# Performance work log

Hardware: AMD Instinct MI355X
Metric: run time of the kernel (lower is better)

## Reference

```python
import jax, jax.numpy as jnp
import numpy as np

CHUNK = 64  # rows of `a` processed per step to bound the [chunk, N, d] abs-diff intermediate
TAIL_K = 4          # selection_tail_size
FAR_K = 64          # far_sample_count
PUSH_K = 4          # pushing_sample_size
HUBER_DELTA = 1.0   # torch.nn.HuberLoss default


def cdist_l1(a, b):
    # a: [M, d], b: [N, d] -> [M, N] Manhattan distances, computed in row chunks
    M, d = a.shape
    def f(a_chunk):  # [CHUNK, d] -> [CHUNK, N]
        return jnp.abs(a_chunk[:, None, :] - b[None, :, :]).sum(-1)
    return jax.lax.map(f, a.reshape(-1, CHUNK, d)).reshape(M, b.shape[0])


def smallest_k_mean(dists, k):
    # mean of the k smallest entries along last dim
    neg_vals, _ = jax.lax.top_k(-dists, k)
    return (-neg_vals).mean(-1)


def huber(x):
    # HuberLoss(pred=x, target=0), delta=1
    ax = jnp.abs(x)
    return jnp.where(ax < HUBER_DELTA, 0.5 * x * x, HUBER_DELTA * (ax - 0.5 * HUBER_DELTA))


def setup_inputs() -> dict:
    key = jax.random.key(0)
    k1, k2 = jax.random.split(key)
    space_samples = jax.random.normal(k1, (2048, 256), dtype=jnp.float32)
    latents = jax.random.normal(k2, (8192, 256), dtype=jnp.float32)
    return {"space_samples": space_samples, "latents": latents}


def reference(space_samples, latents):
    # space_samples: [M, d] drawn from latent_sampler; latents: [N, d]
    space_dists = cdist_l1(space_samples, latents)            # [M, N]
    tail_dists = smallest_k_mean(space_dists, TAIL_K)          # [M]
    far_inds = jax.lax.top_k(tail_dists, FAR_K)[1]             # [FAR_K]
    far_samples = space_samples[far_inds]                      # [FAR_K, d]
    empty_dists = cdist_l1(far_samples, latents)               # [FAR_K, N]
    close_dists = smallest_k_mean(empty_dists, PUSH_K)         # [FAR_K]
    return huber(close_dists).mean()
```

## Files before the change

kernel.cpp:

```cpp
#include <hip/hip_runtime.h>
#include <hip/hip_bf16.h>


static constexpr int M = 2048;
static constexpr int N = 8192;
static constexpr int KQ = 64;
static constexpr int BKQ = 16;
static constexpr int ROWS_PER_BLK = 128;
static constexpr int COLS_PER_BLK = 128;
static constexpr int NCHUNK = N / COLS_PER_BLK;

static constexpr float QS  = 21.0f;
static constexpr float QB  = 126.0f;
static constexpr float INV_QS = 1.0f / 21.0f;

__device__ __forceinline__ float med3f(float a, float b, float c) {
    return __builtin_amdgcn_fmed3f(a, b, c);
}

__device__ __forceinline__ void ins4(float d, float& s0, float& s1, float& s2, float& s3) {
    float n0 = fminf(s0, d);
    float n1 = med3f(s0, s1, d);
    float n2 = med3f(s1, s2, d);
    float n3 = med3f(s2, s3, d);
    s0 = n0; s1 = n1; s2 = n2; s3 = n3;
}

__device__ __forceinline__ unsigned int sad8(unsigned int a, unsigned int b, unsigned int c) {
#if __has_builtin(__builtin_amdgcn_sad_u8)
    return __builtin_amdgcn_sad_u8(a, b, c);
#else
    unsigned int d;
    asm("v_sad_u8 %0, %1, %2, %3" : "=v"(d) : "v"(a), "v"(b), "v"(c));
    return d;
#endif
}

__device__ __forceinline__ unsigned int quant4(const float4 v) {
    const float y0 = fminf(fmaxf(fmaf(v.x, QS, QB), 0.0f), 255.0f);
    const float y1 = fminf(fmaxf(fmaf(v.y, QS, QB), 0.0f), 255.0f);
    const float y2 = fminf(fmaxf(fmaf(v.z, QS, QB), 0.0f), 255.0f);
    const float y3 = fminf(fmaxf(fmaf(v.w, QS, QB), 0.0f), 255.0f);
    const unsigned int b0 = (unsigned int)(int)rintf(y0);
    const unsigned int b1 = (unsigned int)(int)rintf(y1);
    const unsigned int b2 = (unsigned int)(int)rintf(y2);
    const unsigned int b3 = (unsigned int)(int)rintf(y3);
    return b0 | (b1 << 8) | (b2 << 16) | (b3 << 24);
}

__device__ __forceinline__ float huber_pos(float x) {
    const float ax = __builtin_fabsf(x);
    return (ax < 1.0f) ? (0.5f * x * x) : (ax - 0.5f);
}

__global__ __launch_bounds__(256)
void convert_kernel(const float* __restrict__ A, const float* __restrict__ B,
                    unsigned int* __restrict__ At, unsigned int* __restrict__ Bt) {
    __shared__ unsigned int lt[KQ * 65];
    const int tid = threadIdx.x;
    const bool isB = (blockIdx.x < N / 64);
    const float* src = isB ? B : A;
    unsigned int* dst = isB ? Bt : At;
    const int rows = isB ? N : M;
    const int r0 = (isB ? blockIdx.x : (blockIdx.x - N / 64)) * 64;

#pragma unroll
    for (int it = 0; it < 16; ++it) {
        const int qi = it * 256 + tid;
        const int row = qi >> 6;
        const int kq = qi & 63;
        const float4 v = *(const float4*)&src[(r0 + row) * 256 + 4 * kq];
        lt[kq * 65 + row] = quant4(v);
    }
    __syncthreads();
#pragma unroll
    for (int it = 0; it < 16; ++it) {
        const int wi = it * 256 + tid;
        const int row = wi & 63;
        const int kq = wi >> 6;
        dst[(size_t)kq * rows + r0 + row] = lt[kq * 65 + row];
    }
}

__global__ __launch_bounds__(256, 4)
void dist4_kernel(const unsigned int* __restrict__ At, const unsigned int* __restrict__ Bt,
                  float4* __restrict__ ws_dist) {
    __shared__ __align__(16) unsigned int tiles[8192];
    const int tid = threadIdx.x;
    const int tx = tid & 15;
    const int ty = tid >> 4;
    const int bx = blockIdx.x;
    const int by = blockIdx.y;
    const int rowBase = by * ROWS_PER_BLK;
    const int colBase = bx * COLS_PER_BLK;

    const int sKq = tid >> 5;
    const int sC  = (tid & 31) * 4;

    unsigned int acc[8][8];
#pragma unroll
    for (int i = 0; i < 8; ++i)
#pragma unroll
        for (int j = 0; j < 8; ++j) acc[i][j] = 0u;

    uint4 pa0, pa1, pb0, pb1;
    pa0 = *(const uint4*)&At[(sKq) * M + rowBase + sC];
    pa1 = *(const uint4*)&At[(sKq + 8) * M + rowBase + sC];
    pb0 = *(const uint4*)&Bt[(sKq) * N + colBase + sC];
    pb1 = *(const uint4*)&Bt[(sKq + 8) * N + colBase + sC];
    {
        unsigned int* As = tiles;
        unsigned int* Bs = tiles + 2048;
        *(uint4*)&As[sKq * 128 + sC] = pa0;
        *(uint4*)&As[(sKq + 8) * 128 + sC] = pa1;
        *(uint4*)&Bs[sKq * 128 + sC] = pb0;
        *(uint4*)&Bs[(sKq + 8) * 128 + sC] = pb1;
    }

    for (int t0 = 0; t0 < KQ / BKQ; ++t0) {
        __syncthreads();
        if (t0 + 1 < KQ / BKQ) {
            const int kb = (t0 + 1) * BKQ;
            pa0 = *(const uint4*)&At[(kb + sKq) * M + rowBase + sC];
            pa1 = *(const uint4*)&At[(kb + sKq + 8) * M + rowBase + sC];
            pb0 = *(const uint4*)&Bt[(kb + sKq) * N + colBase + sC];
            pb1 = *(const uint4*)&Bt[(kb + sKq + 8) * N + colBase + sC];
        }

        const unsigned int* As = tiles + (t0 & 1) * 4096;
        const unsigned int* Bs = As + 2048;
#pragma unroll 4
        for (int kq = 0; kq < BKQ; ++kq) {
            const uint4 aw0 = *(const uint4*)&As[kq * 128 + 8 * ty];
            const uint4 aw1 = *(const uint4*)&As[kq * 128 + 8 * ty + 4];
            const uint4 bw0 = *(const uint4*)&Bs[kq * 128 + 4 * tx];
            const uint4 bw1 = *(const uint4*)&Bs[kq * 128 + 64 + 4 * tx];
            const unsigned int a[8] = {aw0.x, aw0.y, aw0.z, aw0.w, aw1.x, aw1.y, aw1.z, aw1.w};
            const unsigned int b[8] = {bw0.x, bw0.y, bw0.z, bw0.w, bw1.x, bw1.y, bw1.z, bw1.w};
#pragma unroll
            for (int i = 0; i < 8; ++i) {
#pragma unroll
                for (int j = 0; j < 8; ++j) {
                    acc[i][j] = sad8(a[i], b[j], acc[i][j]);
                }
            }
        }

        if (t0 + 1 < KQ / BKQ) {
            __syncthreads();
            unsigned int* Asw = tiles + ((t0 + 1) & 1) * 4096;
            unsigned int* Bsw = Asw + 2048;
            *(uint4*)&Asw[sKq * 128 + sC] = pa0;
            *(uint4*)&Asw[(sKq + 8) * 128 + sC] = pa1;
            *(uint4*)&Bsw[sKq * 128 + sC] = pb0;
            *(uint4*)&Bsw[(sKq + 8) * 128 + sC] = pb1;
        }
    }

    float s[8][4];
#pragma unroll
    for (int i = 0; i < 8; ++i) {
        float s0 = 1e30f, s1 = 1e30f, s2 = 1e30f, s3 = 1e30f;
#pragma unroll
        for (int j = 0; j < 8; ++j) {
            const float d = (float)acc[i][j] * INV_QS;
            ins4(d, s0, s1, s2, s3);
        }
        s[i][0] = s0; s[i][1] = s1; s[i][2] = s2; s[i][3] = s3;
    }

#pragma unroll
    for (int lvl = 1; lvl <= 8; lvl <<= 1) {
#pragma unroll
        for (int i = 0; i < 8; ++i) {
            const float o0 = __shfl_xor(s[i][0], lvl, 64);
            const float o1 = __shfl_xor(s[i][1], lvl, 64);
            const float o2 = __shfl_xor(s[i][2], lvl, 64);
            const float o3 = __shfl_xor(s[i][3], lvl, 64);
            ins4(o0, s[i][0], s[i][1], s[i][2], s[i][3]);
            ins4(o1, s[i][0], s[i][1], s[i][2], s[i][3]);
            ins4(o2, s[i][0], s[i][1], s[i][2], s[i][3]);
            ins4(o3, s[i][0], s[i][1], s[i][2], s[i][3]);
        }
    }

    if (tx == 0) {
#pragma unroll
        for (int i = 0; i < 8; ++i) {
            ws_dist[bx * M + rowBase + 8 * ty + i] =
                make_float4(s[i][0], s[i][1], s[i][2], s[i][3]);
        }
    }
}

__global__ __launch_bounds__(256)
void tail_kernel(const float4* __restrict__ ws_dist, float* __restrict__ tail) {
    const int gtid = blockIdx.x * 256 + threadIdx.x;
    const int row = gtid >> 3;
    const int q = gtid & 7;
    float s0 = 1e30f, s1 = 1e30f, s2 = 1e30f, s3 = 1e30f;
#pragma unroll
    for (int c = 0; c < 8; ++c) {
        const float4 v = ws_dist[(q * 8 + c) * M + row];
        ins4(v.x, s0, s1, s2, s3);
        ins4(v.y, s0, s1, s2, s3);
        ins4(v.z, s0, s1, s2, s3);
        ins4(v.w, s0, s1, s2, s3);
    }
#pragma unroll
    for (int lvl = 1; lvl <= 4; lvl <<= 1) {
        const float o0 = __shfl_xor(s0, lvl, 64);
        const float o1 = __shfl_xor(s1, lvl, 64);
        const float o2 = __shfl_xor(s2, lvl, 64);
        const float o3 = __shfl_xor(s3, lvl, 64);
        ins4(o0, s0, s1, s2, s3);
        ins4(o1, s0, s1, s2, s3);
        ins4(o2, s0, s1, s2, s3);
        ins4(o3, s0, s1, s2, s3);
    }
    if (q == 0) tail[row] = (s0 + s1 + s2 + s3) * 0.25f;
}

__global__ __launch_bounds__(1024)
void top64_kernel(const float* __restrict__ tail, float* __restrict__ out) {
    __shared__ unsigned int hist[8][256];
    __shared__ unsigned int ctrl[2];
    __shared__ float wsum[16];
    __shared__ unsigned int wcnt[16];
    const int tid = threadIdx.x;
    const int wid = tid >> 6;
    const int lane = tid & 63;

    const unsigned int k0 = __float_as_uint(tail[tid]);
    const unsigned int k1 = __float_as_uint(tail[tid + 1024]);

    if (tid == 0) { ctrl[0] = 0u; ctrl[1] = 64u; }

    for (int p = 0; p < 4; ++p) {
        const int shift = 24 - 8 * p;
        ((unsigned int*)hist)[tid] = 0u;
        ((unsigned int*)hist)[tid + 1024] = 0u;
        __syncthreads();
        const unsigned int prefix = ctrl[0];
        const unsigned int t = ctrl[1];
        bool c0 = true, c1 = true;
        if (p > 0) {
            const int sh8 = shift + 8;
            c0 = ((k0 >> sh8) == (prefix >> sh8));
            c1 = ((k1 >> sh8) == (prefix >> sh8));
        }
        if (c0) atomicAdd(&hist[wid & 7][(k0 >> shift) & 255], 1u);
        if (c1) atomicAdd(&hist[wid & 7][(k1 >> shift) & 255], 1u);
        __syncthreads();
        if (tid < 256) {
            unsigned int h = 0;
#pragma unroll
            for (int r = 0; r < 8; ++r) h += hist[r][tid];
            hist[0][tid] = h;
        }
        __syncthreads();
        if (wid == 0) {
            const unsigned int s4 = hist[0][4 * lane] + hist[0][4 * lane + 1] +
                                    hist[0][4 * lane + 2] + hist[0][4 * lane + 3];
            unsigned int suf = s4;
#pragma unroll
            for (int off = 1; off < 64; off <<= 1) {
                const unsigned int v = __shfl_down(suf, off, 64);
                if (lane + off < 64) suf += v;
            }
            const unsigned long long mask = __ballot(suf >= t);
            const int lstar = 63 - __clzll(mask);
            if (lane == lstar) {
                unsigned int c = suf - s4;
                for (int d = 4 * lstar + 3; d >= 4 * lstar; --d) {
                    const unsigned int cd = hist[0][d];
                    c += cd;
                    if (c >= t) {
                        ctrl[0] = prefix | ((unsigned int)d << shift);
                        ctrl[1] = t - (c - cd);
                        break;
                    }
                }
            }
        }
        __syncthreads();
    }

    const unsigned int T = ctrl[0];
    float sum = 0.0f;
    unsigned int cnt = 0;
    if (k0 > T) { ++cnt; sum += huber_pos(__uint_as_float(k0)); }
    if (k1 > T) { ++cnt; sum += huber_pos(__uint_as_float(k1)); }
#pragma unroll
    for (int off = 32; off > 0; off >>= 1) {
        sum += __shfl_down(sum, off, 64);
        cnt += __shfl_down(cnt, off, 64);
    }
    if (lane == 0) { wsum[wid] = sum; wcnt[wid] = cnt; }
    __syncthreads();
    if (tid == 0) {
        float S = 0.0f;
        unsigned int C = 0;
#pragma unroll
        for (int w = 0; w < 16; ++w) { S += wsum[w]; C += wcnt[w]; }
        const float hT = huber_pos(__uint_as_float(T));
        out[0] = (S + (float)(64u - C) * hT) * (1.0f / 64.0f);
    }
}

extern "C" void kernel_launch(void* const* d_in, const int* in_sizes, int n_in,
                              void* d_out, int out_size, void* d_ws, size_t ws_size,
                              hipStream_t stream) {
    const float* A = (const float*)d_in[0];
    const float* B = (const float*)d_in[1];
    float* out = (float*)d_out;

    unsigned int* Bt = (unsigned int*)d_ws;
    unsigned int* At = (unsigned int*)((char*)d_ws + (size_t)KQ * N * 4);
    float4* ws_dist = (float4*)((char*)d_ws + (size_t)KQ * N * 4 + (size_t)KQ * M * 4);
    float* tail = (float*)((char*)ws_dist + (size_t)NCHUNK * M * sizeof(float4));

    convert_kernel<<<dim3(N / 64 + M / 64), 256, 0, stream>>>(A, B, At, Bt);
    dist4_kernel<<<dim3(NCHUNK, M / ROWS_PER_BLK), 256, 0, stream>>>(At, Bt, ws_dist);
    tail_kernel<<<dim3(M * 8 / 256), 256, 0, stream>>>(ws_dist, tail);
    top64_kernel<<<1, 1024, 0, stream>>>(tail, out);
}
```

Before: 122.4 us.

## Fuse four kernels into one persistent kernel with global atomic barriers

Merges the convert, distance, tail and top-64 kernels into a single launch over 1024 blocks, separated by software grid barriers built on agent-scope atomics, plus a memset to reset the barrier counters. The aim is to remove the launch gaps and tail effects between the four small kernels. The barriers only work if all 1024 blocks are resident at once (256 CUs times 4 blocks per CU), so any shortfall in occupancy would deadlock. Spin waiting and the extra memset also add cost, and the top-64 stage now runs on 256 threads instead of 1024.

```diff
diff --git a/kernel.cpp b/kernel.cpp
--- a/kernel.cpp
+++ b/kernel.cpp
@@ -9,6 +9,7 @@
 static constexpr int ROWS_PER_BLK = 128;
 static constexpr int COLS_PER_BLK = 128;
 static constexpr int NCHUNK = N / COLS_PER_BLK;
+static constexpr int GRID = NCHUNK * (M / ROWS_PER_BLK);
 
 static constexpr float QS  = 21.0f;
 static constexpr float QB  = 126.0f;
@@ -53,258 +54,256 @@
     return (ax < 1.0f) ? (0.5f * x * x) : (ax - 0.5f);
 }
 
-__global__ __launch_bounds__(256)
-void convert_kernel(const float* __restrict__ A, const float* __restrict__ B,
-                    unsigned int* __restrict__ At, unsigned int* __restrict__ Bt) {
-    __shared__ unsigned int lt[KQ * 65];
+__device__ __forceinline__ void gsync(unsigned int* bar) {
+    __syncthreads();
+    if (threadIdx.x == 0) {
+        __hip_atomic_fetch_add(bar, 1u, __ATOMIC_RELEASE, __HIP_MEMORY_SCOPE_AGENT);
+        while (__hip_atomic_load(bar, __ATOMIC_ACQUIRE, __HIP_MEMORY_SCOPE_AGENT) <
+               (unsigned int)GRID) {
+            __builtin_amdgcn_s_sleep(4);
+        }
+    }
+    __syncthreads();
+}
+
+__global__ __launch_bounds__(256, 4)
+void fused_kernel(const float* __restrict__ A, const float* __restrict__ B,
+                  unsigned int* __restrict__ At, unsigned int* __restrict__ Bt,
+                  float4* __restrict__ ws_dist, float* __restrict__ tail,
+                  unsigned int* __restrict__ bars, float* __restrict__ out) {
+    __shared__ __align__(16) unsigned int smem[8192];
     const int tid = threadIdx.x;
-    const bool isB = (blockIdx.x < N / 64);
-    const float* src = isB ? B : A;
-    unsigned int* dst = isB ? Bt : At;
-    const int rows = isB ? N : M;
-    const int r0 = (isB ? blockIdx.x : (blockIdx.x - N / 64)) * 64;
-
-#pragma unroll
-    for (int it = 0; it < 16; ++it) {
-        const int qi = it * 256 + tid;
-        const int row = qi >> 6;
-        const int kq = qi & 63;
-        const float4 v = *(const float4*)&src[(r0 + row) * 256 + 4 * kq];
-        lt[kq * 65 + row] = quant4(v);
-    }
-    __syncthreads();
-#pragma unroll
-    for (int it = 0; it < 16; ++it) {
-        const int wi = it * 256 + tid;
-        const int row = wi & 63;
-        const int kq = wi >> 6;
-        dst[(size_t)kq * rows + r0 + row] = lt[kq * 65 + row];
-    }
-}
-
-__global__ __launch_bounds__(256, 4)
-void dist4_kernel(const unsigned int* __restrict__ At, const unsigned int* __restrict__ Bt,
-                  float4* __restrict__ ws_dist) {
-    __shared__ __align__(16) unsigned int tiles[8192];
-    const int tid = threadIdx.x;
-    const int tx = tid & 15;
-    const int ty = tid >> 4;
-    const int bx = blockIdx.x;
-    const int by = blockIdx.y;
-    const int rowBase = by * ROWS_PER_BLK;
-    const int colBase = bx * COLS_PER_BLK;
-
-    const int sKq = tid >> 5;
-    const int sC  = (tid & 31) * 4;
-
-    unsigned int acc[8][8];
-#pragma unroll
-    for (int i = 0; i < 8; ++i)
-#pragma unroll
-        for (int j = 0; j < 8; ++j) acc[i][j] = 0u;
-
-    uint4 pa0, pa1, pb0, pb1;
-    pa0 = *(const uint4*)&At[(sKq) * M + rowBase + sC];
-    pa1 = *(const uint4*)&At[(sKq + 8) * M + rowBase + sC];
-    pb0 = *(const uint4*)&Bt[(sKq) * N + colBase + sC];
-    pb1 = *(const uint4*)&Bt[(sKq + 8) * N + colBase + sC];
+    const int bid = blockIdx.x;
+
+    if (bid < (N + M) / 64) {
+        const bool isB = bid < N / 64;
+        const float* src = isB ? B : A;
+        unsigned int* dst = isB ? Bt : At;
+        const int rows = isB ? N : M;
+        const int r0 = (isB ? bid : bid - N / 64) * 64;
+#pragma unroll
+        for (int it = 0; it < 16; ++it) {
+            const int qi = it * 256 + tid;
+            const int row = qi >> 6;
+            const int kq = qi & 63;
+            const float4 v = *(const float4*)&src[(r0 + row) * 256 + 4 * kq];
+            smem[kq * 65 + row] = quant4(v);
+        }
+        __syncthreads();
+#pragma unroll
+        for (int it = 0; it < 16; ++it) {
+            const int wi = it * 256 + tid;
+            const int row = wi & 63;
+            const int kq = wi >> 6;
+            dst[(size_t)kq * rows + r0 + row] = smem[kq * 65 + row];
+        }
+    }
+    gsync(&bars[0]);
+
     {
-        unsigned int* As = tiles;
-        unsigned int* Bs = tiles + 2048;
-        *(uint4*)&As[sKq * 128 + sC] = pa0;
-        *(uint4*)&As[(sKq + 8) * 128 + sC] = pa1;
-        *(uint4*)&Bs[sKq * 128 + sC] = pb0;
-        *(uint4*)&Bs[(sKq + 8) * 128 + sC] = pb1;
-    }
-
-    for (int t0 = 0; t0 < KQ / BKQ; ++t0) {
-        __syncthreads();
-        if (t0 + 1 < KQ / BKQ) {
-            const int kb = (t0 + 1) * BKQ;
-            pa0 = *(const uint4*)&At[(kb + sKq) * M + rowBase + sC];
-            pa1 = *(const uint4*)&At[(kb + sKq + 8) * M + rowBase + sC];
-            pb0 = *(const uint4*)&Bt[(kb + sKq) * N + colBase + sC];
-            pb1 = *(const uint4*)&Bt[(kb + sKq + 8) * N + colBase + sC];
-        }
-
-        const unsigned int* As = tiles + (t0 & 1) * 4096;
-        const unsigned int* Bs = As + 2048;
+        unsigned int* tiles = smem;
+        const int tx = tid & 15;
+        const int ty = tid >> 4;
+        const int bx = bid & 63;
+        const int by = bid >> 6;
+        const int rowBase = by * ROWS_PER_BLK;
+        const int colBase = bx * COLS_PER_BLK;
+
+        const int sKq = tid >> 5;
+        const int sC  = (tid & 31) * 4;
+
+        unsigned int acc[8][8];
+#pragma unroll
+        for (int i = 0; i < 8; ++i)
+#pragma unroll
+            for (int j = 0; j < 8; ++j) acc[i][j] = 0u;
+
+        uint4 pa0, pa1, pb0, pb1;
+        pa0 = *(const uint4*)&At[(sKq) * M + rowBase + sC];
+        pa1 = *(const uint4*)&At[(sKq + 8) * M + rowBase + sC];
+        pb0 = *(const uint4*)&Bt[(sKq) * N + colBase + sC];
+        pb1 = *(const uint4*)&Bt[(sKq + 8) * N + colBase + sC];
+        {
+            unsigned int* As = tiles;
+            unsigned int* Bs = tiles + 2048;
+            *(uint4*)&As[sKq * 128 + sC] = pa0;
+            *(uint4*)&As[(sKq + 8) * 128 + sC] = pa1;
+            *(uint4*)&Bs[sKq * 128 + sC] = pb0;
+            *(uint4*)&Bs[(sKq + 8) * 128 + sC] = pb1;
+        }
+
+        for (int t0 = 0; t0 < KQ / BKQ; ++t0) {
+            __syncthreads();
+            if (t0 + 1 < KQ / BKQ) {
+                const int kb = (t0 + 1) * BKQ;
+                pa0 = *(const uint4*)&At[(kb + sKq) * M + rowBase + sC];
+                pa1 = *(const uint4*)&At[(kb + sKq + 8) * M + rowBase + sC];
+                pb0 = *(const uint4*)&Bt[(kb + sKq) * N + colBase + sC];
+                pb1 = *(const uint4*)&Bt[(kb + sKq + 8) * N + colBase + sC];
+            }
+
+            const unsigned int* As = tiles + (t0 & 1) * 4096;
+            const unsigned int* Bs = As + 2048;
 #pragma unroll 4
-        for (int kq = 0; kq < BKQ; ++kq) {
-            const uint4 aw0 = *(const uint4*)&As[kq * 128 + 8 * ty];
-            const uint4 aw1 = *(const uint4*)&As[kq * 128 + 8 * ty + 4];
-            const uint4 bw0 = *(const uint4*)&Bs[kq * 128 + 4 * tx];
-            const uint4 bw1 = *(const uint4*)&Bs[kq * 128 + 64 + 4 * tx];
-            const unsigned int a[8] = {aw0.x, aw0.y, aw0.z, aw0.w, aw1.x, aw1.y, aw1.z, aw1.w};
-            const unsigned int b[8] = {bw0.x, bw0.y, bw0.z, bw0.w, bw1.x, bw1.y, bw1.z, bw1.w};
-#pragma unroll
-            for (int i = 0; i < 8; ++i) {
-#pragma unroll
-                for (int j = 0; j < 8; ++j) {
-                    acc[i][j] = sad8(a[i], b[j], acc[i][j]);
-                }
-            }
-        }
-
-        if (t0 + 1 < KQ / BKQ) {
-            __syncthreads();
-            unsigned int* Asw = tiles + ((t0 + 1) & 1) * 4096;
-            unsigned int* Bsw = Asw + 2048;
-            *(uint4*)&Asw[sKq * 128 + sC] = pa0;
-            *(uint4*)&Asw[(sKq + 8) * 128 + sC] = pa1;
-            *(uint4*)&Bsw[sKq * 128 + sC] = pb0;
-            *(uint4*)&Bsw[(sKq + 8) * 128 + sC] = pb1;
-        }
-    }
-
-    float s[8][4];
-#pragma unroll
-    for (int i = 0; i < 8; ++i) {
-        float s0 = 1e30f, s1 = 1e30f, s2 = 1e30f, s3 = 1e30f;
-#pragma unroll
-        for (int j = 0; j < 8; ++j) {
-            const float d = (float)acc[i][j] * INV_QS;
-            ins4(d, s0, s1, s2, s3);
-        }
-        s[i][0] = s0; s[i][1] = s1; s[i][2] = s2; s[i][3] = s3;
-    }
-
-#pragma unroll
-    for (int lvl = 1; lvl <= 8; lvl <<= 1) {
-#pragma unroll
-        for (int i = 0; i < 8; ++i) {
-            const float o0 = __shfl_xor(s[i][0], lvl, 64);
-            const float o1 = __shfl_xor(s[i][1], lvl, 64);
-            const float o2 = __shfl_xor(s[i][2], lvl, 64);
-            const float o3 = __shfl_xor(s[i][3], lvl, 64);
-            ins4(o0, s[i][0], s[i][1], s[i][2], s[i][3]);
-            ins4(o1, s[i][0], s[i][1], s[i][2], s[i][3]);
-            ins4(o2, s[i][0], s[i][1], s[i][2], s[i][3]);
-            ins4(o3, s[i][0], s[i][1], s[i][2], s[i][3]);
-        }
-    }
-
-    if (tx == 0) {
-#pragma unroll
-        for (int i = 0; i < 8; ++i) {
-            ws_dist[bx * M + rowBase + 8 * ty + i] =
-                make_float4(s[i][0], s[i][1], s[i][2], s[i][3]);
-        }
-    }
-}
-
-__global__ __launch_bounds__(256)
-void tail_kernel(const float4* __restrict__ ws_dist, float* __restrict__ tail) {
-    const int gtid = blockIdx.x * 256 + threadIdx.x;
-    const int row = gtid >> 3;
-    const int q = gtid & 7;
-    float s0 = 1e30f, s1 = 1e30f, s2 = 1e30f, s3 = 1e30f;
-#pragma unroll
-    for (int c = 0; c < 8; ++c) {
-        const float4 v = ws_dist[(q * 8 + c) * M + row];
-        ins4(v.x, s0, s1, s2, s3);
-        ins4(v.y, s0, s1, s2, s3);
-        ins4(v.z, s0, s1, s2, s3);
-        ins4(v.w, s0, s1, s2, s3);
-    }
-#pragma unroll
-    for (int lvl = 1; lvl <= 4; lvl <<= 1) {
-        const float o0 = __shfl_xor(s0, lvl, 64);
-        const float o1 = __shfl_xor(s1, lvl, 64);
-        const float o2 = __shfl_xor(s2, lvl, 64);
-        const float o3 = __shfl_xor(s3, lvl, 64);
-        ins4(o0, s0, s1, s2, s3);
-        ins4(o1, s0, s1, s2, s3);
-        ins4(o2, s0, s1, s2, s3);
-        ins4(o3, s0, s1, s2, s3);
-    }
-    if (q == 0) tail[row] = (s0 + s1 + s2 + s3) * 0.25f;
-}
-
-__global__ __launch_bounds__(1024)
-void top64_kernel(const float* __restrict__ tail, float* __restrict__ out) {
-    __shared__ unsigned int hist[8][256];
-    __shared__ unsigned int ctrl[2];
-    __shared__ float wsum[16];
-    __shared__ unsigned int wcnt[16];
-    const int tid = threadIdx.x;
-    const int wid = tid >> 6;
-    const int lane = tid & 63;
-
-    const unsigned int k0 = __float_as_uint(tail[tid]);
-    const unsigned int k1 = __float_as_uint(tail[tid + 1024]);
-
-    if (tid == 0) { ctrl[0] = 0u; ctrl[1] = 64u; }
-
-    for (int p = 0; p < 4; ++p) {
-        const int shift = 24 - 8 * p;
-        ((unsigned int*)hist)[tid] = 0u;
-        ((unsigned int*)hist)[tid + 1024] = 0u;
-        __syncthreads();
-        const unsigned int prefix = ctrl[0];
-        const unsigned int t = ctrl[1];
-        bool c0 = true, c1 = true;
-        if (p > 0) {
-            const int sh8 = shift + 8;
-            c0 = ((k0 >> sh8) == (prefix >> sh8));
-            c1 = ((k1 >> sh8) == (prefix >> sh8));
-        }
-        if (c0) atomicAdd(&hist[wid & 7][(k0 >> shift) & 255], 1u);
-        if (c1) atomicAdd(&hist[wid & 7][(k1 >> shift) & 255], 1u);
-        __syncthreads();
-        if (tid < 256) {
-            unsigned int h = 0;
-#pragma unroll
-            for (int r = 0; r < 8; ++r) h += hist[r][tid];
-            hist[0][tid] = h;
-        }
-        __syncthreads();
-        if (wid == 0) {
-            const unsigned int s4 = hist[0][4 * lane] + hist[0][4 * lane + 1] +
-                                    hist[0][4 * lane + 2] + hist[0][4 * lane + 3];
-            unsigned int suf = s4;
-#pragma unroll
-            for (int off = 1; off < 64; off <<= 1) {
-                const unsigned int v = __shfl_down(suf, off, 64);
-                if (lane + off < 64) suf += v;
-            }
-            const unsigned long long mask = __ballot(suf >= t);
-            const int lstar = 63 - __clzll(mask);
-            if (lane == lstar) {
-                unsigned int c = suf - s4;
-                for (int d = 4 * lstar + 3; d >= 4 * lstar; --d) {
-                    const unsigned int cd = hist[0][d];
-                    c += cd;
-                    if (c >= t) {
-                        ctrl[0] = prefix | ((unsigned int)d << shift);
-                        ctrl[1] = t - (c - cd);
-                        break;
+            for (int kq = 0; kq < BKQ; ++kq) {
+                const uint4 aw0 = *(const uint4*)&As[kq * 128 + 8 * ty];
+                const uint4 aw1 = *(const uint4*)&As[kq * 128 + 8 * ty + 4];
+                const uint4 bw0 = *(const uint4*)&Bs[kq * 128 + 4 * tx];
+                const uint4 bw1 = *(const uint4*)&Bs[kq * 128 + 64 + 4 * tx];
+                const unsigned int a[8] = {aw0.x, aw0.y, aw0.z, aw0.w, aw1.x, aw1.y, aw1.z, aw1.w};
+                const unsigned int b[8] = {bw0.x, bw0.y, bw0.z, bw0.w, bw1.x, bw1.y, bw1.z, bw1.w};
+#pragma unroll
+                for (int i = 0; i < 8; ++i) {
+#pragma unroll
+                    for (int j = 0; j < 8; ++j) {
+                        acc[i][j] = sad8(a[i], b[j], acc[i][j]);
                     }
                 }
             }
-        }
+
+            if (t0 + 1 < KQ / BKQ) {
+                __syncthreads();
+                unsigned int* Asw = tiles + ((t0 + 1) & 1) * 4096;
+                unsigned int* Bsw = Asw + 2048;
+                *(uint4*)&Asw[sKq * 128 + sC] = pa0;
+                *(uint4*)&Asw[(sKq + 8) * 128 + sC] = pa1;
+                *(uint4*)&Bsw[sKq * 128 + sC] = pb0;
+                *(uint4*)&Bsw[(sKq + 8) * 128 + sC] = pb1;
+            }
+        }
+
+#pragma unroll
+        for (int i = 0; i < 8; ++i) {
+            float s0 = 1e30f, s1 = 1e30f, s2 = 1e30f, s3 = 1e30f;
+#pragma unroll
+            for (int j = 0; j < 8; ++j) {
+                ins4((float)acc[i][j] * INV_QS, s0, s1, s2, s3);
+            }
+#pragma unroll
+            for (int lvl = 1; lvl <= 8; lvl <<= 1) {
+                const float o0 = __shfl_xor(s0, lvl, 64);
+                const float o1 = __shfl_xor(s1, lvl, 64);
+                const float o2 = __shfl_xor(s2, lvl, 64);
+                const float o3 = __shfl_xor(s3, lvl, 64);
+                ins4(o0, s0, s1, s2, s3);
+                ins4(o1, s0, s1, s2, s3);
+                ins4(o2, s0, s1, s2, s3);
+                ins4(o3, s0, s1, s2, s3);
+            }
+            if (tx == 0) {
+                ws_dist[bx * M + rowBase + 8 * ty + i] = make_float4(s0, s1, s2, s3);
+            }
+        }
+    }
+    gsync(&bars[1]);
+
+    if (bid < 64) {
+        const int gtid = bid * 256 + tid;
+        const int row = gtid >> 3;
+        const int q = gtid & 7;
+        float s0 = 1e30f, s1 = 1e30f, s2 = 1e30f, s3 = 1e30f;
+#pragma unroll
+        for (int c = 0; c < 8; ++c) {
+            const float4 v = ws_dist[(q * 8 + c) * M + row];
+            ins4(v.x, s0, s1, s2, s3);
+            ins4(v.y, s0, s1, s2, s3);
+            ins4(v.z, s0, s1, s2, s3);
+            ins4(v.w, s0, s1, s2, s3);
+        }
+#pragma unroll
+        for (int lvl = 1; lvl <= 4; lvl <<= 1) {
+            const float o0 = __shfl_xor(s0, lvl, 64);
+            const float o1 = __shfl_xor(s1, lvl, 64);
+            const float o2 = __shfl_xor(s2, lvl, 64);
+            const float o3 = __shfl_xor(s3, lvl, 64);
+            ins4(o0, s0, s1, s2, s3);
+            ins4(o1, s0, s1, s2, s3);
+            ins4(o2, s0, s1, s2, s3);
+            ins4(o3, s0, s1, s2, s3);
+        }
+        if (q == 0) tail[row] = (s0 + s1 + s2 + s3) * 0.25f;
+    }
+    gsync(&bars[2]);
+
+    if (bid == 0) {
+        unsigned int* hist = smem;
+        unsigned int* ctrl = smem + 1024;
+        float* wsum = (float*)(smem + 1028);
+        unsigned int* wcnt = smem + 1032;
+        const int wid = tid >> 6;
+        const int lane = tid & 63;
+
+        unsigned int k[8];
+#pragma unroll
+        for (int j = 0; j < 8; ++j) k[j] = __float_as_uint(tail[j * 256 + tid]);
+
+        if (tid == 0) { ctrl[0] = 0u; ctrl[1] = 64u; }
+
+        for (int p = 0; p < 4; ++p) {
+            const int shift = 24 - 8 * p;
+#pragma unroll
+            for (int z = 0; z < 4; ++z) hist[z * 256 + tid] = 0u;
+            __syncthreads();
+            const unsigned int prefix = ctrl[0];
+            const unsigned int t = ctrl[1];
+            const int sh8 = shift + 8;
+#pragma unroll
+            for (int j = 0; j < 8; ++j) {
+                const bool c = (p == 0) || ((k[j] >> sh8) == (prefix >> sh8));
+                if (c) atomicAdd(&hist[wid * 256 + ((k[j] >> shift) & 255)], 1u);
+            }
+            __syncthreads();
+            const unsigned int h = hist[tid] + hist[256 + tid] +
+                                   hist[512 + tid] + hist[768 + tid];
+            hist[tid] = h;
+            __syncthreads();
+            if (tid < 64) {
+                const unsigned int s4 = hist[4 * lane] + hist[4 * lane + 1] +
+                                        hist[4 * lane + 2] + hist[4 * lane + 3];
+                unsigned int suf = s4;
+#pragma unroll
+                for (int off = 1; off < 64; off <<= 1) {
+                    const unsigned int v = __shfl_down(suf, off, 64);
+                    if (lane + off < 64) suf += v;
+                }
+                const unsigned long long mask = __ballot(suf >= t);
+                const int lstar = 63 - __clzll(mask);
+                if (lane == lstar) {
+                    unsigned int c = suf - s4;
+                    for (int d = 4 * lstar + 3; d >= 4 * lstar; --d) {
+                        const unsigned int cd = hist[d];
+                        c += cd;
+                        if (c >= t) {
+                            ctrl[0] = prefix | ((unsigned int)d << shift);
+                            ctrl[1] = t - (c - cd);
+                            break;
+                        }
+                    }
+                }
+            }
+            __syncthreads();
+        }
+
+        const unsigned int T = ctrl[0];
+        float sum = 0.0f;
+        unsigned int cnt = 0;
+#pragma unroll
+        for (int j = 0; j < 8; ++j) {
+            if (k[j] > T) { ++cnt; sum += huber_pos(__uint_as_float(k[j])); }
+        }
+#pragma unroll
+        for (int off = 32; off > 0; off >>= 1) {
+            sum += __shfl_down(sum, off, 64);
+            cnt += __shfl_down(cnt, off, 64);
+        }
+        if (lane == 0) { wsum[wid] = sum; wcnt[wid] = cnt; }
         __syncthreads();
-    }
-
-    const unsigned int T = ctrl[0];
-    float sum = 0.0f;
-    unsigned int cnt = 0;
-    if (k0 > T) { ++cnt; sum += huber_pos(__uint_as_float(k0)); }
-    if (k1 > T) { ++cnt; sum += huber_pos(__uint_as_float(k1)); }
-#pragma unroll
-    for (int off = 32; off > 0; off >>= 1) {
-        sum += __shfl_down(sum, off, 64);
-        cnt += __shfl_down(cnt, off, 64);
-    }
-    if (lane == 0) { wsum[wid] = sum; wcnt[wid] = cnt; }
-    __syncthreads();
-    if (tid == 0) {
-        float S = 0.0f;
-        unsigned int C = 0;
-#pragma unroll
-        for (int w = 0; w < 16; ++w) { S += wsum[w]; C += wcnt[w]; }
-        const float hT = huber_pos(__uint_as_float(T));
-        out[0] = (S + (float)(64u - C) * hT) * (1.0f / 64.0f);
+        if (tid == 0) {
+            const float S = wsum[0] + wsum[1] + wsum[2] + wsum[3];
+            const unsigned int C = wcnt[0] + wcnt[1] + wcnt[2] + wcnt[3];
+            const float hT = huber_pos(__uint_as_float(T));
+            out[0] = (S + (float)(64u - C) * hT) * (1.0f / 64.0f);
+        }
     }
 }
 
@@ -319,9 +318,8 @@
     unsigned int* At = (unsigned int*)((char*)d_ws + (size_t)KQ * N * 4);
     float4* ws_dist = (float4*)((char*)d_ws + (size_t)KQ * N * 4 + (size_t)KQ * M * 4);
     float* tail = (float*)((char*)ws_dist + (size_t)NCHUNK * M * sizeof(float4));
-
-    convert_kernel<<<dim3(N / 64 + M / 64), 256, 0, stream>>>(A, B, At, Bt);
-    dist4_kernel<<<dim3(NCHUNK, M / ROWS_PER_BLK), 256, 0, stream>>>(At, Bt, ws_dist);
-    tail_kernel<<<dim3(M * 8 / 256), 256, 0, stream>>>(ws_dist, tail);
-    top64_kernel<<<1, 1024, 0, stream>>>(tail, out);
-}
+    unsigned int* bars = (unsigned int*)(tail + M);
+
+    hipMemsetAsync(bars, 0, 3 * sizeof(unsigned int), stream);
+    fused_kernel<<<dim3(GRID), dim3(256), 0, stream>>>(A, B, At, Bt, ws_dist, tail, bars, out);
+}
```

After: 450.9 us. 3.68x slower.
